# Kernel tuning notes

Measured on AMD Instinct MI355X. Metric: run time of the kernel, lower is better.

## Reference

```python
import jax, jax.numpy as jnp
import numpy as np

HEAD = 16
EMB = 1024
D_K = EMB // HEAD


def setup_inputs() -> dict:
    key = jax.random.key(0)
    ks = jax.random.split(key, 11)
    B, S, E = 2, 2048, EMB
    scale = 1.0 / np.sqrt(E)
    inp = {
        "query": jax.random.normal(ks[0], (B, S, E), jnp.float32),
        "key": jax.random.normal(ks[1], (B, S, E), jnp.float32),
        "value": jax.random.normal(ks[2], (B, S, E), jnp.float32),
        "Wq": jax.random.normal(ks[3], (E, E), jnp.float32) * scale,
        "bq": jnp.zeros((E,), jnp.float32),
        "Wk": jax.random.normal(ks[4], (E, E), jnp.float32) * scale,
        "bk": jnp.zeros((E,), jnp.float32),
        "Wv": jax.random.normal(ks[5], (E, E), jnp.float32) * scale,
        "bv": jnp.zeros((E,), jnp.float32),
        "Wo": jax.random.normal(ks[6], (E, E), jnp.float32) * scale,
        "bo": jnp.zeros((E,), jnp.float32),
    }
    return inp


def reference(query, key, value, Wq, bq, Wk, bk, Wv, bv, Wo, bo):
    B, S, E = query.shape
    # 3 input projections, split into heads: [B, H, S, d_k]
    def proj(x, W, b):
        return (x @ W.T + b).reshape(B, S, HEAD, D_K).transpose(0, 2, 1, 3)

    q = proj(query, Wq, bq)
    k = proj(key, Wk, bk)
    v = proj(value, Wv, bv)

    # scaled dot-product attention (full matrix, as in original)
    scores = jnp.einsum("bhqd,bhkd->bhqk", q, k) / jnp.sqrt(jnp.float32(D_K))
    attn = jax.nn.softmax(scores, axis=-1)  # dropout in eval mode = identity
    x = jnp.einsum("bhqk,bhkd->bhqd", attn, v)

    # merge heads and output projection
    x = x.transpose(0, 2, 1, 3).reshape(B, S, E)
    return x @ Wo.T + bo
```

## Files before the change

### kernel.cpp

```cpp
#include <hip/hip_runtime.h>
#include <hip/hip_bf16.h>
#include <math.h>


constexpr int Sn = 2048;
constexpr int En = 1024;
constexpr int Hn = 16;
constexpr int Dk = 64;
constexpr int Kn = 1024;
constexpr size_t WSZ = 1048576;
constexpr size_t TSZ = 4194304;

typedef __bf16 bf16x8 __attribute__((ext_vector_type(8)));
typedef float  f32x4  __attribute__((ext_vector_type(4)));

union U16 { uint4 u; bf16x8 v; __hip_bfloat16 h[8]; };
union U8  { uint2 u; __hip_bfloat16 h[4]; };

__device__ inline U16 cvt8f(const float* __restrict__ p) {
    float4 a = *(const float4*)p;
    float4 b = *(const float4*)(p + 4);
    U16 r;
    r.h[0] = __float2bfloat16(a.x); r.h[1] = __float2bfloat16(a.y);
    r.h[2] = __float2bfloat16(a.z); r.h[3] = __float2bfloat16(a.w);
    r.h[4] = __float2bfloat16(b.x); r.h[5] = __float2bfloat16(b.y);
    r.h[6] = __float2bfloat16(b.z); r.h[7] = __float2bfloat16(b.w);
    return r;
}

__device__ inline void gload16(const __hip_bfloat16* g, __hip_bfloat16* l) {
    __builtin_amdgcn_global_load_lds(
        (const __attribute__((address_space(1))) void*)g,
        (__attribute__((address_space(3))) void*)l, 16, 0, 0);
}

template<int ROWS, int NW>
__device__ inline void stage_tile(const __hip_bfloat16* __restrict__ src, int ld,
                                  __hip_bfloat16* lds, int w, int lane) {
    int l8 = lane >> 3;
    int g = (lane & 7) ^ (l8 & 7);
    #pragma unroll
    for (int j = 0; j < ROWS / (8 * NW); ++j) {
        int c = j * NW + w;
        gload16(src + (size_t)(c * 8 + l8) * ld + g * 8, lds + c * 512);
    }
}

__global__ __launch_bounds__(256)
void cvt_w(const float* __restrict__ w0, const float* __restrict__ w1,
           const float* __restrict__ w2, const float* __restrict__ w3,
           __hip_bfloat16* __restrict__ dst)
{
    int y = blockIdx.y;
    const float* src = (y == 0) ? w0 : (y == 1) ? w1 : (y == 2) ? w2 : w3;
    size_t i = ((size_t)blockIdx.x * 256 + threadIdx.x) * 8;
    U16 r = cvt8f(src + i);
    *(uint4*)&dst[(size_t)y * WSZ + i] = r.u;
}

__global__ __launch_bounds__(256)
void qkv_gemm(const float* __restrict__ xq, const float* __restrict__ xk,
              const float* __restrict__ xv, const __hip_bfloat16* __restrict__ Wbf,
              const float* __restrict__ bq, const float* __restrict__ bk,
              const float* __restrict__ bv,
              __hip_bfloat16* __restrict__ Qw, __hip_bfloat16* __restrict__ Kw,
              __hip_bfloat16* __restrict__ Vtw)
{
    __shared__ __align__(16) __hip_bfloat16 As[64 * 64];
    __shared__ __align__(16) __hip_bfloat16 Bs[128 * 64];

    const int tid = threadIdx.x, w = tid >> 6, lane = tid & 63;
    const int l15 = lane & 15, lg = lane >> 4, l7 = lane & 7;
    const int z = blockIdx.z;
    const float* A    = (z == 0) ? xq : (z == 1) ? xk : xv;
    const float* bias = (z == 0) ? bq : (z == 1) ? bk : bv;
    const __hip_bfloat16* W = Wbf + (size_t)z * WSZ;
    const int blockM = blockIdx.x * 64, blockN = blockIdx.y * 128;
    const int wm = (w & 1) * 32, wn = (w >> 1) * 64;

    const int arow = tid >> 2, acb = tid & 3;
    const int coff0 = ((0 * 4 + lg) ^ l7) * 8;
    const int coff1 = ((1 * 4 + lg) ^ l7) * 8;

    f32x4 acc[2][4];
    #pragma unroll
    for (int i = 0; i < 2; ++i)
        #pragma unroll
        for (int j = 0; j < 4; ++j) acc[i][j] = {0.f, 0.f, 0.f, 0.f};

    for (int k0 = 0; k0 < Kn; k0 += 64) {
        {
            const float* ap = A + (size_t)(blockM + arow) * Kn + k0 + acb * 16;
            U16 r0 = cvt8f(ap);
            U16 r1 = cvt8f(ap + 8);
            int s7 = arow & 7, g0 = acb * 2;
            *(uint4*)&As[arow * 64 + ((g0 ^ s7) * 8)]       = r0.u;
            *(uint4*)&As[arow * 64 + (((g0 + 1) ^ s7) * 8)] = r1.u;
        }
        stage_tile<128, 4>(W + (size_t)blockN * Kn + k0, Kn, Bs, w, lane);
        __syncthreads();

        U16 af[2][2], bf[4][2];
        #pragma unroll
        for (int mt = 0; mt < 2; ++mt) {
            int r = (wm + mt * 16 + l15) * 64;
            af[mt][0].u = *(const uint4*)&As[r + coff0];
            af[mt][1].u = *(const uint4*)&As[r + coff1];
        }
        #pragma unroll
        for (int nt = 0; nt < 4; ++nt) {
            int r = (wn + nt * 16 + l15) * 64;
            bf[nt][0].u = *(const uint4*)&Bs[r + coff0];
            bf[nt][1].u = *(const uint4*)&Bs[r + coff1];
        }
        #pragma unroll
        for (int mt = 0; mt < 2; ++mt)
            #pragma unroll
            for (int nt = 0; nt < 4; ++nt) {
                acc[mt][nt] = __builtin_amdgcn_mfma_f32_16x16x32_bf16(af[mt][0].v, bf[nt][0].v, acc[mt][nt], 0, 0, 0);
                acc[mt][nt] = __builtin_amdgcn_mfma_f32_16x16x32_bf16(af[mt][1].v, bf[nt][1].v, acc[mt][nt], 0, 0, 0);
            }
        __syncthreads();
    }

    #pragma unroll
    for (int nt = 0; nt < 4; ++nt) {
        int n = blockN + wn + nt * 16 + l15;
        float bvn = bias[n];
        int h_ = n >> 6, d_ = n & 63;
        #pragma unroll
        for (int mt = 0; mt < 2; ++mt) {
            int m0 = blockM + wm + mt * 16 + lg * 4;
            int b_ = m0 >> 11, s_ = m0 & (Sn - 1);
            if (z == 2) {
                U8 pk;
                #pragma unroll
                for (int i = 0; i < 4; ++i) pk.h[i] = __float2bfloat16(acc[mt][nt][i] + bvn);
                *(uint2*)&Vtw[(((size_t)b_ * Hn + h_) * Dk + d_) * Sn + s_] = pk.u;
            } else {
                __hip_bfloat16* D = (z == 0) ? Qw : Kw;
                #pragma unroll
                for (int i = 0; i < 4; ++i)
                    D[(((size_t)b_ * Hn + h_) * Sn + s_ + i) * Dk + d_] =
                        __float2bfloat16(acc[mt][nt][i] + bvn);
            }
        }
    }
}

__global__ __launch_bounds__(256)
void fin_gemm(const __hip_bfloat16* __restrict__ A, const __hip_bfloat16* __restrict__ W,
              const float* __restrict__ bias, float* __restrict__ out)
{
    __shared__ __align__(16) __hip_bfloat16 As[64 * 64];
    __shared__ __align__(16) __hip_bfloat16 Bs[128 * 64];

    const int tid = threadIdx.x, w = tid >> 6, lane = tid & 63;
    const int l15 = lane & 15, lg = lane >> 4, l7 = lane & 7;
    const int blockM = blockIdx.x * 64, blockN = blockIdx.y * 128;
    const int wm = (w & 1) * 32, wn = (w >> 1) * 64;
    const int coff0 = (lg ^ l7) * 8;
    const int coff1 = ((4 + lg) ^ l7) * 8;

    f32x4 acc[2][4];
    #pragma unroll
    for (int i = 0; i < 2; ++i)
        #pragma unroll
        for (int j = 0; j < 4; ++j) acc[i][j] = {0.f, 0.f, 0.f, 0.f};

    for (int k0 = 0; k0 < Kn; k0 += 64) {
        stage_tile<64, 4>(A + (size_t)blockM * Kn + k0, Kn, As, w, lane);
        stage_tile<128, 4>(W + (size_t)blockN * Kn + k0, Kn, Bs, w, lane);
        __syncthreads();

        U16 af[2][2], bf[4][2];
        #pragma unroll
        for (int mt = 0; mt < 2; ++mt) {
            int r = (wm + mt * 16 + l15) * 64;
            af[mt][0].u = *(const uint4*)&As[r + coff0];
            af[mt][1].u = *(const uint4*)&As[r + coff1];
        }
        #pragma unroll
        for (int nt = 0; nt < 4; ++nt) {
            int r = (wn + nt * 16 + l15) * 64;
            bf[nt][0].u = *(const uint4*)&Bs[r + coff0];
            bf[nt][1].u = *(const uint4*)&Bs[r + coff1];
        }
        #pragma unroll
        for (int mt = 0; mt < 2; ++mt)
            #pragma unroll
            for (int nt = 0; nt < 4; ++nt) {
                acc[mt][nt] = __builtin_amdgcn_mfma_f32_16x16x32_bf16(af[mt][0].v, bf[nt][0].v, acc[mt][nt], 0, 0, 0);
                acc[mt][nt] = __builtin_amdgcn_mfma_f32_16x16x32_bf16(af[mt][1].v, bf[nt][1].v, acc[mt][nt], 0, 0, 0);
            }
        __syncthreads();
    }

    #pragma unroll
    for (int nt = 0; nt < 4; ++nt) {
        int n = blockN + wn + nt * 16 + l15;
        float bvn = bias[n];
        #pragma unroll
        for (int mt = 0; mt < 2; ++mt) {
            int m0 = blockM + wm + mt * 16 + lg * 4;
            #pragma unroll
            for (int i = 0; i < 4; ++i)
                out[(size_t)(m0 + i) * Kn + n] = acc[mt][nt][i] + bvn;
        }
    }
}

__global__ __launch_bounds__(128)
void attn(const __hip_bfloat16* __restrict__ Q, const __hip_bfloat16* __restrict__ K,
          const __hip_bfloat16* __restrict__ Vt, __hip_bfloat16* __restrict__ X)
{
    __shared__ __align__(16) __hip_bfloat16 Ks[64 * 64];
    __shared__ __align__(16) __hip_bfloat16 Vts[64 * 64];
    __shared__ __align__(16) float Ps[64][68];

    const int bh = blockIdx.y, q0 = blockIdx.x * 64;
    const int tid = threadIdx.x, w = tid >> 6, lane = tid & 63;
    const int l15 = lane & 15, lg = lane >> 4, l7 = lane & 7;
    const int coff0 = (lg ^ l7) * 8;
    const int coff1 = ((4 + lg) ^ l7) * 8;

    const __hip_bfloat16* Qb = Q  + (size_t)bh * Sn * Dk;
    const __hip_bfloat16* Kb = K  + (size_t)bh * Sn * Dk;
    const __hip_bfloat16* Vb = Vt + (size_t)bh * Dk * Sn;

    U16 aq[2][2];
    #pragma unroll
    for (int mt = 0; mt < 2; ++mt) {
        const __hip_bfloat16* qp = Qb + (size_t)(q0 + w * 32 + mt * 16 + l15) * Dk + lg * 8;
        aq[mt][0].u = *(const uint4*)qp;
        aq[mt][1].u = *(const uint4*)(qp + 32);
    }

    f32x4 o[2][4];
    float lpart[2][4];
    #pragma unroll
    for (int mt = 0; mt < 2; ++mt)
        #pragma unroll
        for (int j = 0; j < 4; ++j) { o[mt][j] = {0.f, 0.f, 0.f, 0.f}; lpart[mt][j] = 0.f; }

    for (int k0 = 0; k0 < Sn; k0 += 64) {
        stage_tile<64, 2>(Kb + (size_t)k0 * Dk, Dk, Ks, w, lane);
        stage_tile<64, 2>(Vb + k0, Sn, Vts, w, lane);
        __syncthreads();

        f32x4 s[2][4];
        #pragma unroll
        for (int nt = 0; nt < 4; ++nt) {
            int r = (nt * 16 + l15) * 64;
            U16 b0, b1;
            b0.u = *(const uint4*)&Ks[r + coff0];
            b1.u = *(const uint4*)&Ks[r + coff1];
            #pragma unroll
            for (int mt = 0; mt < 2; ++mt) {
                f32x4 a = {0.f, 0.f, 0.f, 0.f};
                a = __builtin_amdgcn_mfma_f32_16x16x32_bf16(aq[mt][0].v, b0.v, a, 0, 0, 0);
                a = __builtin_amdgcn_mfma_f32_16x16x32_bf16(aq[mt][1].v, b1.v, a, 0, 0, 0);
                s[mt][nt] = a;
            }
        }

        #pragma unroll
        for (int mt = 0; mt < 2; ++mt)
            #pragma unroll
            for (int nt = 0; nt < 4; ++nt)
                #pragma unroll
                for (int i = 0; i < 4; ++i) {
                    float p = __expf(s[mt][nt][i] * 0.125f);
                    lpart[mt][i] += p;
                    Ps[w * 32 + mt * 16 + lg * 4 + i][nt * 16 + l15] = p;
                }

        U16 pf[2][2];
        #pragma unroll
        for (int mt = 0; mt < 2; ++mt) {
            const float* pr = &Ps[w * 32 + mt * 16 + l15][lg * 8];
            pf[mt][0] = cvt8f(pr);
            pf[mt][1] = cvt8f(pr + 32);
        }
        #pragma unroll
        for (int dt = 0; dt < 4; ++dt) {
            int r = (dt * 16 + l15) * 64;
            U16 v0, v1;
            v0.u = *(const uint4*)&Vts[r + coff0];
            v1.u = *(const uint4*)&Vts[r + coff1];
            #pragma unroll
            for (int mt = 0; mt < 2; ++mt) {
                o[mt][dt] = __builtin_amdgcn_mfma_f32_16x16x32_bf16(pf[mt][0].v, v0.v, o[mt][dt], 0, 0, 0);
                o[mt][dt] = __builtin_amdgcn_mfma_f32_16x16x32_bf16(pf[mt][1].v, v1.v, o[mt][dt], 0, 0, 0);
            }
        }
        __syncthreads();
    }

    #pragma unroll
    for (int mt = 0; mt < 2; ++mt)
        #pragma unroll
        for (int i = 0; i < 4; ++i) {
            float v = lpart[mt][i];
            #pragma unroll
            for (int off = 1; off < 16; off <<= 1) v += __shfl_xor(v, off, 64);
            lpart[mt][i] = 1.f / v;
        }

    int b_ = bh >> 4, h_ = bh & (Hn - 1);
    #pragma unroll
    for (int mt = 0; mt < 2; ++mt)
        #pragma unroll
        for (int i = 0; i < 4; ++i) {
            int sr = q0 + w * 32 + mt * 16 + lg * 4 + i;
            __hip_bfloat16* xp = X + ((size_t)(b_ * Sn + sr)) * En + h_ * Dk + l15;
            #pragma unroll
            for (int dt = 0; dt < 4; ++dt)
                xp[dt * 16] = __float2bfloat16(o[mt][dt][i] * lpart[mt][i]);
        }
}

extern "C" void kernel_launch(void* const* d_in, const int* in_sizes, int n_in,
                              void* d_out, int out_size, void* d_ws, size_t ws_size,
                              hipStream_t stream)
{
    const float* query = (const float*)d_in[0];
    const float* key   = (const float*)d_in[1];
    const float* value = (const float*)d_in[2];
    const float* Wq = (const float*)d_in[3];
    const float* bq = (const float*)d_in[4];
    const float* Wk = (const float*)d_in[5];
    const float* bk = (const float*)d_in[6];
    const float* Wv = (const float*)d_in[7];
    const float* bv = (const float*)d_in[8];
    const float* Wo = (const float*)d_in[9];
    const float* bo = (const float*)d_in[10];
    float* out = (float*)d_out;

    __hip_bfloat16* Wbf = (__hip_bfloat16*)d_ws;
    __hip_bfloat16* Qw  = Wbf + 4 * WSZ;
    __hip_bfloat16* Kw  = Qw + TSZ;
    __hip_bfloat16* Vtw = Kw + TSZ;
    __hip_bfloat16* Xw  = Vtw + TSZ;

    cvt_w<<<dim3(512, 4), 256, 0, stream>>>(Wq, Wk, Wv, Wo, Wbf);
    qkv_gemm<<<dim3(64, 8, 3), 256, 0, stream>>>(query, key, value, Wbf,
                                                 bq, bk, bv, Qw, Kw, Vtw);
    attn<<<dim3(Sn / 64, 32), 128, 0, stream>>>(Qw, Kw, Vtw, Xw);
    fin_gemm<<<dim3(64, 8), 256, 0, stream>>>(Xw, Wbf + 3 * WSZ, bo, out);
}
```

Before: 254.4 us.

## Enlarge GEMM tiles to 128x128 and restructure attention with bf16 P and 4 warps

Both GEMMs move from 64x128 to 128x128 block tiles, so each warp computes a 64x64 sub-tile and the block count is halved. This raises reuse of each staged tile at the cost of more accumulator registers. The attention kernel now uses 4 warps over 128 queries, so each staged K/V tile is shared by twice as many rows. It computes S transposed (K times Q), writes P to LDS as packed bf16 instead of fp32, and uses a cheaper shuffle reduction for the row sums. Fewer blocks may reduce occupancy and the GPU's ability to hide latency.

After: 272.5 us. 1.07x slower.

```diff
diff --git a/kernel.cpp b/kernel.cpp
--- a/kernel.cpp
+++ b/kernel.cpp
@@ -10,12 +10,13 @@
 constexpr int Kn = 1024;
 constexpr size_t WSZ = 1048576;
 constexpr size_t TSZ = 4194304;
+constexpr int PST = 72;
 
 typedef __bf16 bf16x8 __attribute__((ext_vector_type(8)));
 typedef float  f32x4  __attribute__((ext_vector_type(4)));
 
 union U16 { uint4 u; bf16x8 v; __hip_bfloat16 h[8]; };
-union U8  { uint2 u; __hip_bfloat16 h[4]; };
+union U8  { uint2 u; __hip_bfloat162 h2[2]; __hip_bfloat16 h[4]; };
 
 __device__ inline U16 cvt8f(const float* __restrict__ p) {
     float4 a = *(const float4*)p;
@@ -66,7 +67,7 @@
               __hip_bfloat16* __restrict__ Qw, __hip_bfloat16* __restrict__ Kw,
               __hip_bfloat16* __restrict__ Vtw)
 {
-    __shared__ __align__(16) __hip_bfloat16 As[64 * 64];
+    __shared__ __align__(16) __hip_bfloat16 As[128 * 64];
     __shared__ __align__(16) __hip_bfloat16 Bs[128 * 64];
 
     const int tid = threadIdx.x, w = tid >> 6, lane = tid & 63;
@@ -75,34 +76,35 @@
     const float* A    = (z == 0) ? xq : (z == 1) ? xk : xv;
     const float* bias = (z == 0) ? bq : (z == 1) ? bk : bv;
     const __hip_bfloat16* W = Wbf + (size_t)z * WSZ;
-    const int blockM = blockIdx.x * 64, blockN = blockIdx.y * 128;
-    const int wm = (w & 1) * 32, wn = (w >> 1) * 64;
-
-    const int arow = tid >> 2, acb = tid & 3;
-    const int coff0 = ((0 * 4 + lg) ^ l7) * 8;
-    const int coff1 = ((1 * 4 + lg) ^ l7) * 8;
-
-    f32x4 acc[2][4];
-    #pragma unroll
-    for (int i = 0; i < 2; ++i)
+    const int blockM = blockIdx.x * 128, blockN = blockIdx.y * 128;
+    const int wm = (w & 1) * 64, wn = (w >> 1) * 64;
+
+    const int arow = tid >> 1, acb = (tid & 1) * 4;
+    const int coff0 = (lg ^ l7) * 8;
+    const int coff1 = ((4 + lg) ^ l7) * 8;
+
+    f32x4 acc[4][4];
+    #pragma unroll
+    for (int i = 0; i < 4; ++i)
         #pragma unroll
         for (int j = 0; j < 4; ++j) acc[i][j] = {0.f, 0.f, 0.f, 0.f};
 
     for (int k0 = 0; k0 < Kn; k0 += 64) {
         {
-            const float* ap = A + (size_t)(blockM + arow) * Kn + k0 + acb * 16;
-            U16 r0 = cvt8f(ap);
-            U16 r1 = cvt8f(ap + 8);
-            int s7 = arow & 7, g0 = acb * 2;
-            *(uint4*)&As[arow * 64 + ((g0 ^ s7) * 8)]       = r0.u;
-            *(uint4*)&As[arow * 64 + (((g0 + 1) ^ s7) * 8)] = r1.u;
+            const float* ap = A + (size_t)(blockM + arow) * Kn + k0 + acb * 8;
+            int s7 = arow & 7;
+            #pragma unroll
+            for (int g = 0; g < 4; ++g) {
+                U16 r = cvt8f(ap + g * 8);
+                *(uint4*)&As[arow * 64 + (((acb + g) ^ s7) * 8)] = r.u;
+            }
         }
         stage_tile<128, 4>(W + (size_t)blockN * Kn + k0, Kn, Bs, w, lane);
         __syncthreads();
 
-        U16 af[2][2], bf[4][2];
-        #pragma unroll
-        for (int mt = 0; mt < 2; ++mt) {
+        U16 af[4][2], bf[4][2];
+        #pragma unroll
+        for (int mt = 0; mt < 4; ++mt) {
             int r = (wm + mt * 16 + l15) * 64;
             af[mt][0].u = *(const uint4*)&As[r + coff0];
             af[mt][1].u = *(const uint4*)&As[r + coff1];
@@ -114,7 +116,7 @@
             bf[nt][1].u = *(const uint4*)&Bs[r + coff1];
         }
         #pragma unroll
-        for (int mt = 0; mt < 2; ++mt)
+        for (int mt = 0; mt < 4; ++mt)
             #pragma unroll
             for (int nt = 0; nt < 4; ++nt) {
                 acc[mt][nt] = __builtin_amdgcn_mfma_f32_16x16x32_bf16(af[mt][0].v, bf[nt][0].v, acc[mt][nt], 0, 0, 0);
@@ -129,7 +131,7 @@
         float bvn = bias[n];
         int h_ = n >> 6, d_ = n & 63;
         #pragma unroll
-        for (int mt = 0; mt < 2; ++mt) {
+        for (int mt = 0; mt < 4; ++mt) {
             int m0 = blockM + wm + mt * 16 + lg * 4;
             int b_ = m0 >> 11, s_ = m0 & (Sn - 1);
             if (z == 2) {
@@ -152,30 +154,30 @@
 void fin_gemm(const __hip_bfloat16* __restrict__ A, const __hip_bfloat16* __restrict__ W,
               const float* __restrict__ bias, float* __restrict__ out)
 {
-    __shared__ __align__(16) __hip_bfloat16 As[64 * 64];
+    __shared__ __align__(16) __hip_bfloat16 As[128 * 64];
     __shared__ __align__(16) __hip_bfloat16 Bs[128 * 64];
 
     const int tid = threadIdx.x, w = tid >> 6, lane = tid & 63;
     const int l15 = lane & 15, lg = lane >> 4, l7 = lane & 7;
-    const int blockM = blockIdx.x * 64, blockN = blockIdx.y * 128;
-    const int wm = (w & 1) * 32, wn = (w >> 1) * 64;
+    const int blockM = blockIdx.x * 128, blockN = blockIdx.y * 128;
+    const int wm = (w & 1) * 64, wn = (w >> 1) * 64;
     const int coff0 = (lg ^ l7) * 8;
     const int coff1 = ((4 + lg) ^ l7) * 8;
 
-    f32x4 acc[2][4];
-    #pragma unroll
-    for (int i = 0; i < 2; ++i)
+    f32x4 acc[4][4];
+    #pragma unroll
+    for (int i = 0; i < 4; ++i)
         #pragma unroll
         for (int j = 0; j < 4; ++j) acc[i][j] = {0.f, 0.f, 0.f, 0.f};
 
     for (int k0 = 0; k0 < Kn; k0 += 64) {
-        stage_tile<64, 4>(A + (size_t)blockM * Kn + k0, Kn, As, w, lane);
+        stage_tile<128, 4>(A + (size_t)blockM * Kn + k0, Kn, As, w, lane);
         stage_tile<128, 4>(W + (size_t)blockN * Kn + k0, Kn, Bs, w, lane);
         __syncthreads();
 
-        U16 af[2][2], bf[4][2];
-        #pragma unroll
-        for (int mt = 0; mt < 2; ++mt) {
+        U16 af[4][2], bf[4][2];
+        #pragma unroll
+        for (int mt = 0; mt < 4; ++mt) {
             int r = (wm + mt * 16 + l15) * 64;
             af[mt][0].u = *(const uint4*)&As[r + coff0];
             af[mt][1].u = *(const uint4*)&As[r + coff1];
@@ -187,7 +189,7 @@
             bf[nt][1].u = *(const uint4*)&Bs[r + coff1];
         }
         #pragma unroll
-        for (int mt = 0; mt < 2; ++mt)
+        for (int mt = 0; mt < 4; ++mt)
             #pragma unroll
             for (int nt = 0; nt < 4; ++nt) {
                 acc[mt][nt] = __builtin_amdgcn_mfma_f32_16x16x32_bf16(af[mt][0].v, bf[nt][0].v, acc[mt][nt], 0, 0, 0);
@@ -201,7 +203,7 @@
         int n = blockN + wn + nt * 16 + l15;
         float bvn = bias[n];
         #pragma unroll
-        for (int mt = 0; mt < 2; ++mt) {
+        for (int mt = 0; mt < 4; ++mt) {
             int m0 = blockM + wm + mt * 16 + lg * 4;
             #pragma unroll
             for (int i = 0; i < 4; ++i)
@@ -210,15 +212,15 @@
     }
 }
 
-__global__ __launch_bounds__(128)
+__global__ __launch_bounds__(256)
 void attn(const __hip_bfloat16* __restrict__ Q, const __hip_bfloat16* __restrict__ K,
           const __hip_bfloat16* __restrict__ Vt, __hip_bfloat16* __restrict__ X)
 {
     __shared__ __align__(16) __hip_bfloat16 Ks[64 * 64];
     __shared__ __align__(16) __hip_bfloat16 Vts[64 * 64];
-    __shared__ __align__(16) float Ps[64][68];
-
-    const int bh = blockIdx.y, q0 = blockIdx.x * 64;
+    __shared__ __align__(16) __hip_bfloat16 Ps[128 * PST];
+
+    const int bh = blockIdx.y, q0 = blockIdx.x * 128;
     const int tid = threadIdx.x, w = tid >> 6, lane = tid & 63;
     const int l15 = lane & 15, lg = lane >> 4, l7 = lane & 7;
     const int coff0 = (lg ^ l7) * 8;
@@ -230,93 +232,95 @@
 
     U16 aq[2][2];
     #pragma unroll
-    for (int mt = 0; mt < 2; ++mt) {
-        const __hip_bfloat16* qp = Qb + (size_t)(q0 + w * 32 + mt * 16 + l15) * Dk + lg * 8;
-        aq[mt][0].u = *(const uint4*)qp;
-        aq[mt][1].u = *(const uint4*)(qp + 32);
+    for (int qt = 0; qt < 2; ++qt) {
+        const __hip_bfloat16* qp = Qb + (size_t)(q0 + w * 32 + qt * 16 + l15) * Dk + lg * 8;
+        aq[qt][0].u = *(const uint4*)qp;
+        aq[qt][1].u = *(const uint4*)(qp + 32);
     }
 
     f32x4 o[2][4];
-    float lpart[2][4];
-    #pragma unroll
-    for (int mt = 0; mt < 2; ++mt)
-        #pragma unroll
-        for (int j = 0; j < 4; ++j) { o[mt][j] = {0.f, 0.f, 0.f, 0.f}; lpart[mt][j] = 0.f; }
+    float lpart[2];
+    #pragma unroll
+    for (int qt = 0; qt < 2; ++qt) {
+        lpart[qt] = 0.f;
+        #pragma unroll
+        for (int dt = 0; dt < 4; ++dt) o[qt][dt] = {0.f, 0.f, 0.f, 0.f};
+    }
+
+    __hip_bfloat16* Pw = Ps + (w * 32) * PST;
 
     for (int k0 = 0; k0 < Sn; k0 += 64) {
-        stage_tile<64, 2>(Kb + (size_t)k0 * Dk, Dk, Ks, w, lane);
-        stage_tile<64, 2>(Vb + k0, Sn, Vts, w, lane);
-        __syncthreads();
-
-        f32x4 s[2][4];
-        #pragma unroll
-        for (int nt = 0; nt < 4; ++nt) {
-            int r = (nt * 16 + l15) * 64;
-            U16 b0, b1;
-            b0.u = *(const uint4*)&Ks[r + coff0];
-            b1.u = *(const uint4*)&Ks[r + coff1];
-            #pragma unroll
-            for (int mt = 0; mt < 2; ++mt) {
-                f32x4 a = {0.f, 0.f, 0.f, 0.f};
-                a = __builtin_amdgcn_mfma_f32_16x16x32_bf16(aq[mt][0].v, b0.v, a, 0, 0, 0);
-                a = __builtin_amdgcn_mfma_f32_16x16x32_bf16(aq[mt][1].v, b1.v, a, 0, 0, 0);
-                s[mt][nt] = a;
-            }
-        }
-
-        #pragma unroll
-        for (int mt = 0; mt < 2; ++mt)
-            #pragma unroll
-            for (int nt = 0; nt < 4; ++nt)
-                #pragma unroll
-                for (int i = 0; i < 4; ++i) {
-                    float p = __expf(s[mt][nt][i] * 0.125f);
-                    lpart[mt][i] += p;
-                    Ps[w * 32 + mt * 16 + lg * 4 + i][nt * 16 + l15] = p;
-                }
-
-        U16 pf[2][2];
-        #pragma unroll
-        for (int mt = 0; mt < 2; ++mt) {
-            const float* pr = &Ps[w * 32 + mt * 16 + l15][lg * 8];
-            pf[mt][0] = cvt8f(pr);
-            pf[mt][1] = cvt8f(pr + 32);
+        stage_tile<64, 4>(Kb + (size_t)k0 * Dk, Dk, Ks, w, lane);
+        stage_tile<64, 4>(Vb + k0, Sn, Vts, w, lane);
+        __syncthreads();
+
+        U16 kf[4][2];
+        #pragma unroll
+        for (int kt = 0; kt < 4; ++kt) {
+            int r = (kt * 16 + l15) * 64;
+            kf[kt][0].u = *(const uint4*)&Ks[r + coff0];
+            kf[kt][1].u = *(const uint4*)&Ks[r + coff1];
+        }
+        #pragma unroll
+        for (int kt = 0; kt < 4; ++kt)
+            #pragma unroll
+            for (int qt = 0; qt < 2; ++qt) {
+                f32x4 s = {0.f, 0.f, 0.f, 0.f};
+                s = __builtin_amdgcn_mfma_f32_16x16x32_bf16(kf[kt][0].v, aq[qt][0].v, s, 0, 0, 0);
+                s = __builtin_amdgcn_mfma_f32_16x16x32_bf16(kf[kt][1].v, aq[qt][1].v, s, 0, 0, 0);
+                float p0 = __expf(s[0] * 0.125f), p1 = __expf(s[1] * 0.125f);
+                float p2 = __expf(s[2] * 0.125f), p3 = __expf(s[3] * 0.125f);
+                lpart[qt] += (p0 + p1) + (p2 + p3);
+                U8 pk;
+                pk.h2[0] = __float22bfloat162_rn({p0, p1});
+                pk.h2[1] = __float22bfloat162_rn({p2, p3});
+                *(uint2*)&Pw[(qt * 16 + l15) * PST + kt * 16 + lg * 4] = pk.u;
+            }
+
+        U16 pf[2][2], vf[4][2];
+        #pragma unroll
+        for (int qt = 0; qt < 2; ++qt) {
+            const __hip_bfloat16* pr = &Pw[(qt * 16 + l15) * PST + lg * 8];
+            pf[qt][0].u = *(const uint4*)pr;
+            pf[qt][1].u = *(const uint4*)(pr + 32);
         }
         #pragma unroll
         for (int dt = 0; dt < 4; ++dt) {
             int r = (dt * 16 + l15) * 64;
-            U16 v0, v1;
-            v0.u = *(const uint4*)&Vts[r + coff0];
-            v1.u = *(const uint4*)&Vts[r + coff1];
-            #pragma unroll
-            for (int mt = 0; mt < 2; ++mt) {
-                o[mt][dt] = __builtin_amdgcn_mfma_f32_16x16x32_bf16(pf[mt][0].v, v0.v, o[mt][dt], 0, 0, 0);
-                o[mt][dt] = __builtin_amdgcn_mfma_f32_16x16x32_bf16(pf[mt][1].v, v1.v, o[mt][dt], 0, 0, 0);
-            }
-        }
-        __syncthreads();
-    }
-
-    #pragma unroll
-    for (int mt = 0; mt < 2; ++mt)
+            vf[dt][0].u = *(const uint4*)&Vts[r + coff0];
+            vf[dt][1].u = *(const uint4*)&Vts[r + coff1];
+        }
+        #pragma unroll
+        for (int qt = 0; qt < 2; ++qt)
+            #pragma unroll
+            for (int dt = 0; dt < 4; ++dt) {
+                o[qt][dt] = __builtin_amdgcn_mfma_f32_16x16x32_bf16(pf[qt][0].v, vf[dt][0].v, o[qt][dt], 0, 0, 0);
+                o[qt][dt] = __builtin_amdgcn_mfma_f32_16x16x32_bf16(pf[qt][1].v, vf[dt][1].v, o[qt][dt], 0, 0, 0);
+            }
+        __syncthreads();
+    }
+
+    float linv[2][4];
+    #pragma unroll
+    for (int qt = 0; qt < 2; ++qt) {
+        float v = lpart[qt];
+        v += __shfl_xor(v, 16, 64);
+        v += __shfl_xor(v, 32, 64);
+        #pragma unroll
+        for (int i = 0; i < 4; ++i)
+            linv[qt][i] = 1.f / __shfl(v, lg * 4 + i, 16);
+    }
+
+    int b_ = bh >> 4, h_ = bh & (Hn - 1);
+    #pragma unroll
+    for (int qt = 0; qt < 2; ++qt)
         #pragma unroll
         for (int i = 0; i < 4; ++i) {
-            float v = lpart[mt][i];
-            #pragma unroll
-            for (int off = 1; off < 16; off <<= 1) v += __shfl_xor(v, off, 64);
-            lpart[mt][i] = 1.f / v;
-        }
-
-    int b_ = bh >> 4, h_ = bh & (Hn - 1);
-    #pragma unroll
-    for (int mt = 0; mt < 2; ++mt)
-        #pragma unroll
-        for (int i = 0; i < 4; ++i) {
-            int sr = q0 + w * 32 + mt * 16 + lg * 4 + i;
+            int sr = q0 + w * 32 + qt * 16 + lg * 4 + i;
             __hip_bfloat16* xp = X + ((size_t)(b_ * Sn + sr)) * En + h_ * Dk + l15;
             #pragma unroll
             for (int dt = 0; dt < 4; ++dt)
-                xp[dt * 16] = __float2bfloat16(o[mt][dt][i] * lpart[mt][i]);
+                xp[dt * 16] = __float2bfloat16(o[qt][dt][i] * linv[qt][i]);
         }
 }
 
@@ -344,8 +348,8 @@
     __hip_bfloat16* Xw  = Vtw + TSZ;
 
     cvt_w<<<dim3(512, 4), 256, 0, stream>>>(Wq, Wk, Wv, Wo, Wbf);
-    qkv_gemm<<<dim3(64, 8, 3), 256, 0, stream>>>(query, key, value, Wbf,
+    qkv_gemm<<<dim3(32, 8, 3), 256, 0, stream>>>(query, key, value, Wbf,
                                                  bq, bk, bv, Qw, Kw, Vtw);
-    attn<<<dim3(Sn / 64, 32), 128, 0, stream>>>(Qw, Kw, Vtw, Xw);
-    fin_gemm<<<dim3(64, 8), 256, 0, stream>>>(Xw, Wbf + 3 * WSZ, bo, out);
-}
+    attn<<<dim3(Sn / 128, 32), 256, 0, stream>>>(Qw, Kw, Vtw, Xw);
+    fin_gemm<<<dim3(32, 8), 256, 0, stream>>>(Xw, Wbf + 3 * WSZ, bo, out);
+}
```
